# Optimization experiments

Measured on AMD Instinct MI355X. Metric: run time of the kernel, lower is better.

Reference implementation:

```python
import jax, jax.numpy as jnp
import numpy as np

H, KV, D, HID = 32, 8, 128, 4096
B, S = 1, 2048
ROPE_THETA = 10000.0


def setup_inputs() -> dict:
    key = jax.random.key(0)
    ks = jax.random.split(key, 5)
    std = 0.02
    return {
        "x": jax.random.normal(ks[0], (B, S, HID), jnp.float32),
        "Wq": jax.random.normal(ks[1], (H * D, HID), jnp.float32) * std,
        "Wk": jax.random.normal(ks[2], (KV * D, HID), jnp.float32) * std,
        "Wv": jax.random.normal(ks[3], (KV * D, HID), jnp.float32) * std,
        "Wo": jax.random.normal(ks[4], (HID, H * D), jnp.float32) * std,
    }


def _rope_cos_sin(seq_len, dim, dtype):
    inv_freq = 1.0 / (ROPE_THETA ** (jnp.arange(0, dim, 2, dtype=jnp.float32) / dim))
    t = jnp.arange(seq_len, dtype=jnp.float32)
    freqs = jnp.einsum("s,d->sd", t, inv_freq)          # [S, D/2]
    emb = jnp.concatenate([freqs, freqs], axis=-1)        # [S, D]
    return jnp.cos(emb).astype(dtype), jnp.sin(emb).astype(dtype)


def _rotate_half(x):
    x1, x2 = jnp.split(x, 2, axis=-1)
    return jnp.concatenate([-x2, x1], axis=-1)


def reference(x, Wq, Wk, Wv, Wo):
    Bx, Sx, _ = x.shape
    q = (x @ Wq.T).reshape(Bx, Sx, H, D).transpose(0, 2, 1, 3)    # [B,H,S,D]
    k = (x @ Wk.T).reshape(Bx, Sx, KV, D).transpose(0, 2, 1, 3)   # [B,KV,S,D]
    v = (x @ Wv.T).reshape(Bx, Sx, KV, D).transpose(0, 2, 1, 3)

    cos, sin = _rope_cos_sin(Sx, D, x.dtype)                       # [S,D]
    q = q * cos + _rotate_half(q) * sin
    k = k * cos + _rotate_half(k) * sin

    rep = H // KV
    k = jnp.repeat(k, rep, axis=1)                                 # [B,H,S,D]
    v = jnp.repeat(v, rep, axis=1)

    scale = 1.0 / jnp.sqrt(jnp.asarray(D, x.dtype))
    scores = jnp.einsum("bhqd,bhkd->bhqk", q, k) * scale           # [B,H,S,S]
    causal = jnp.tril(jnp.ones((Sx, Sx), dtype=bool))
    scores = jnp.where(causal, scores, jnp.asarray(-1e30, x.dtype))
    attn = jax.nn.softmax(scores, axis=-1)
    out = jnp.einsum("bhqk,bhkd->bhqd", attn, v)                   # [B,H,S,D]
    out = out.transpose(0, 2, 1, 3).reshape(Bx, Sx, H * D)
    return out @ Wo.T
```

## Files before the change

kernel.cpp:

```cpp
#include <hip/hip_runtime.h>

typedef unsigned short u16;
typedef unsigned int u32;

using f32x4  = __attribute__((ext_vector_type(4))) float;
using f32x16 = __attribute__((ext_vector_type(16))) float;
using bf16x8 = __attribute__((ext_vector_type(8))) __bf16;

#define S_LEN 2048
#define HID_DIM 4096
#define NH 32
#define NKV 8
#define HD 128
#define QKVN 6144

__device__ __forceinline__ u16 f2b(float f) {
  union { float f; u32 u; } v; v.f = f;
  u32 r = (v.u + 0x7FFFu + ((v.u >> 16) & 1u)) >> 16;
  return (u16)r;
}
__device__ __forceinline__ float b2f(u16 b) {
  union { u32 u; float f; } v; v.u = ((u32)b) << 16;
  return v.f;
}

__device__ __forceinline__ u32 cvtpk_bf16(float lo, float hi) {
  u32 r;
  asm("v_cvt_pk_bf16_f32 %0, %1, %2" : "=v"(r) : "v"(lo), "v"(hi));
  return r;
}
__device__ __forceinline__ void plane_swap(u32& a, u32& b) {
  asm volatile("v_permlane32_swap_b32 %0, %1" : "+v"(a), "+v"(b));
}

#define AS1 __attribute__((address_space(1)))
#define AS3 __attribute__((address_space(3)))
__device__ __forceinline__ void gl_lds16(const u16* g, u16* l) {
  __builtin_amdgcn_global_load_lds((const AS1 u32*)g, (AS3 u32*)l, 16, 0, 0);
}

#define SBAR  __builtin_amdgcn_s_barrier()
#define SCHED0 __builtin_amdgcn_sched_barrier(0)
#define LGKM0 do { asm volatile("s_waitcnt lgkmcnt(0)" ::: "memory"); SCHED0; } while (0)
#define PRIO1 __builtin_amdgcn_s_setprio(1)
#define PRIO0 __builtin_amdgcn_s_setprio(0)

template <int N> __device__ __forceinline__ void waitv() {
  if constexpr (N == 0)      asm volatile("s_waitcnt vmcnt(0)" ::: "memory");
  else if constexpr (N == 4) asm volatile("s_waitcnt vmcnt(4)" ::: "memory");
  else if constexpr (N == 5) asm volatile("s_waitcnt vmcnt(5)" ::: "memory");
  else if constexpr (N == 6) asm volatile("s_waitcnt vmcnt(6)" ::: "memory");
  else if constexpr (N == 7) asm volatile("s_waitcnt vmcnt(7)" ::: "memory");
  else                       asm volatile("s_waitcnt vmcnt(0)" ::: "memory");
  SCHED0;
}

#define X4T 2097152
#define Q4T 4194304
#define K4T 1048576
#define TOT4 (X4T + Q4T + K4T + K4T + Q4T)
__global__ void cast_all(const float* __restrict__ x,  const float* __restrict__ wq,
                         const float* __restrict__ wk, const float* __restrict__ wv,
                         const float* __restrict__ wo,
                         u16* __restrict__ xb, u16* __restrict__ wqkv,
                         u16* __restrict__ wo_b) {
  int i = blockIdx.x * blockDim.x + threadIdx.x;
  int stride = gridDim.x * blockDim.x;
  for (; i < TOT4; i += stride) {
    const float* src;
    uint2* dst;
    int off;
    if (i < X4T)                     { src = x;  dst = (uint2*)xb;   off = i; }
    else if (i < X4T + Q4T)          { src = wq; dst = (uint2*)wqkv; off = i - X4T; }
    else if (i < X4T + Q4T + K4T)    { src = wk; dst = (uint2*)wqkv + Q4T; off = i - X4T - Q4T; }
    else if (i < X4T + Q4T + 2*K4T)  { src = wv; dst = (uint2*)wqkv + Q4T + K4T; off = i - X4T - Q4T - K4T; }
    else                             { src = wo; dst = (uint2*)wo_b; off = i - X4T - Q4T - 2*K4T; }
    float4 v = ((const float4*)src)[off];
    uint2 o;
    o.x = (u32)f2b(v.x) | ((u32)f2b(v.y) << 16);
    o.y = (u32)f2b(v.z) | ((u32)f2b(v.w) << 16);
    dst[off] = o;
  }
}

#define STAGE(DST, SRC, CH, LDK)                                   \
  _Pragma("unroll") for (int c = 0; c < (CH); ++c) {               \
    int d_ = c * 8192 + tid * 16;                                  \
    int rw_ = d_ >> 7;                                             \
    int cb_ = (d_ & 127) ^ ((rw_ & 7) << 4);                       \
    gl_lds16((SRC) + (size_t)rw_ * (LDK) + (cb_ >> 1), (DST) + (d_ >> 1)); \
  }

#define RDA(ABUF, MLO, KS)                                                    \
  _Pragma("unroll") for (int mm = 0; mm < 4; ++mm)                            \
    af[(MLO) + mm][KS] = *(const bf16x8*)((const char*)(ABUF) +               \
      (wmo + ((MLO) + mm) * 16 + lr) * 128 + (((((KS) << 2) | lg) ^ lr7) << 4));

#define RDB(BBUF, KS)                                                         \
  _Pragma("unroll") for (int nn = 0; nn < NF; ++nn)                           \
    bfr[nn][KS] = *(const bf16x8*)((const char*)(BBUF) +                      \
      (wno + nn * 16 + lr) * 128 + (((((KS) << 2) | lg) ^ lr7) << 4));

#define MFMA_Q(MLO, KS)                                                       \
  _Pragma("unroll") for (int mm = 0; mm < 4; ++mm)                            \
  _Pragma("unroll") for (int nn = 0; nn < NF; ++nn)                           \
    acc[(MLO) + mm][nn] = __builtin_amdgcn_mfma_f32_16x16x32_bf16(            \
        af[(MLO) + mm][KS], bfr[nn][KS], acc[(MLO) + mm][nn], 0, 0, 0);

template <int BM, int BN, int WN, int CBF>
__global__ __launch_bounds__(512, 4) void gemm8p(
    const u16* __restrict__ A, const u16* __restrict__ B, void* __restrict__ Cout,
    int M, int N, int K)
{
  constexpr int MF = BM / 32;
  constexpr int NF = WN / 16;
  constexpr int LA = BM / 64;
  constexpr int LB = BN / 64;
  constexpr int LT = LA + LB;
  extern __shared__ __align__(16) u16 smem[];
  u16* const As0 = smem;
  u16* const Bs0 = smem + 2 * BM * 64;

  const int tid  = threadIdx.x;
  const int lane = tid & 63;
  const int wave = tid >> 6;
  const int lr  = lane & 15;
  const int lg  = lane >> 4;
  const int lr7 = lane & 7;

  const int nbx = N / BN;
  const int bid = blockIdx.x;
  const int cpx = gridDim.x >> 3;
  const int swz = (bid & 7) * cpx + (bid >> 3);
  const int bm = (swz / nbx) * BM;
  const int bn = (swz % nbx) * BN;
  const int wmo = (wave >> 2) * (BM / 2);
  const int wno = (wave & 3) * WN;

  const int NT = K >> 6;

  f32x4 acc[MF][NF] = {};
  bf16x8 af[MF][2], bfr[NF][2];

  const u16* aP = A + (size_t)bm * K;
  const u16* bP = B + (size_t)bn * K;

  STAGE(As0,           aP,      LA, K);
  STAGE(Bs0,           bP,      LB, K);
  STAGE(As0 + BM * 64, aP + 64, LA, K);
  STAGE(Bs0 + BN * 64, bP + 64, LB, K);
  waitv<LT>();
  SBAR; SCHED0;

  for (int t = 0; t < NT; ++t) {
    const int buf = t & 1;
    const u16* ab = As0 + buf * (BM * 64);
    const u16* bb = Bs0 + buf * (BN * 64);
    const bool st = (t + 2 < NT);

    RDA(ab, 0, 0);
    if constexpr (MF == 8) { RDA(ab, 4, 0); }
    RDB(bb, 0);
    LGKM0;
    PRIO1; MFMA_Q(0, 0); if constexpr (MF == 8) { MFMA_Q(4, 0); } PRIO0;
    RDA(ab, 0, 1);
    if constexpr (MF == 8) { RDA(ab, 4, 1); }
    RDB(bb, 1);
    LGKM0;
    SBAR;

    if (st) {
      STAGE(As0 + buf * (BM * 64), aP + (size_t)(t + 2) * 64, LA, K);
      STAGE(Bs0 + buf * (BN * 64), bP + (size_t)(t + 2) * 64, LB, K);
    }
    PRIO1; MFMA_Q(0, 1); if constexpr (MF == 8) { MFMA_Q(4, 1); } PRIO0;
    if (t + 1 < NT) {
      if (st) waitv<LT>(); else waitv<0>();
    }
    SBAR; SCHED0;
  }

#pragma unroll
  for (int m = 0; m < MF; ++m)
#pragma unroll
    for (int j = 0; j < 4; ++j) {
      int row = bm + wmo + m * 16 + lg * 4 + j;
      size_t base = (size_t)row * N + bn + wno + lr;
      if constexpr (CBF) {
        u16* C = (u16*)Cout;
#pragma unroll
        for (int nn = 0; nn < NF; ++nn) C[base + nn * 16] = f2b(acc[m][nn][j]);
      } else {
        float* C = (float*)Cout;
#pragma unroll
        for (int nn = 0; nn < NF; ++nn) C[base + nn * 16] = acc[m][nn][j];
      }
    }
}

__global__ void rope_qk(const u16* __restrict__ qkv, u16* __restrict__ dst,
                        int col_off, float scale, int frag) {
  int idx = blockIdx.x * blockDim.x + threadIdx.x;
  int i = idx & 63;
  int s = (idx >> 6) & (S_LEN - 1);
  int h = idx >> 17;
  const u16* row = qkv + (size_t)s * QKVN + col_off + h * HD;
  float a = b2f(row[i]);
  float b = b2f(row[i + 64]);
  float invf = __expf(-(float)i * 0.14391156831212787f);
  float f = (float)s * invf;
  float sn, cs;
  sincosf(f, &sn, &cs);
  float o1 = (a * cs - b * sn) * scale;
  float o2 = (b * cs + a * sn) * scale;
  if (frag) {
    int qt = h * 64 + (s >> 5);
    int qq = s & 31;
    int i2 = i + 64;
    dst[((qt * 8 + (i  >> 4)) * 2 + ((i  >> 3) & 1)) * 256 + qq * 8 + (i  & 7)] = f2b(o1);
    dst[((qt * 8 + (i2 >> 4)) * 2 + ((i2 >> 3) & 1)) * 256 + qq * 8 + (i2 & 7)] = f2b(o2);
  } else {
    u16* orow = dst + ((size_t)h * S_LEN + s) * HD;
    orow[i]      = f2b(o1);
    orow[i + 64] = f2b(o2);
  }
}

__global__ __launch_bounds__(256) void vf_pack(const u16* __restrict__ qkv,
                                               u16* __restrict__ VF) {
  __shared__ u16 vlds[32][136];
  const int bid = blockIdx.x;
  const int kv = bid >> 6, t = bid & 63;
  const int tid = threadIdx.x;
  const int r = tid >> 3, d0 = (tid & 7) * 16;
  const u16* src = qkv + (size_t)(t * 32 + r) * QKVN + 5120 + kv * HD + d0;
  *(bf16x8*)&vlds[r][d0]     = *(const bf16x8*)src;
  *(bf16x8*)&vlds[r][d0 + 8] = *(const bf16x8*)(src + 8);
  __syncthreads();
  u16* outt = VF + (size_t)bid * 4096;
#pragma unroll
  for (int g = 0; g < 2; ++g) {
    int G = tid + g * 256;
    int q = G & 31, dt = (G >> 5) & 3, hi2 = (G >> 7) & 1, kc = G >> 8;
    union { u16 u[8]; uint4 v; } o;
#pragma unroll
    for (int e = 0; e < 8; ++e)
      o.u[e] = vlds[kc * 16 + hi2 * 8 + e][dt * 32 + q];
    *(uint4*)&outt[G * 8] = o.v;
  }
}

__global__ __launch_bounds__(256, 2) void attn_fwd(
    const u16* __restrict__ QF,
    const u16* __restrict__ KF,
    const u16* __restrict__ VF,
    u16* __restrict__ Out)
{
  const int tid  = threadIdx.x;
  const int lane = tid & 63;
  const int wv   = tid >> 6;
  const int q31  = lane & 31;
  const int hi   = lane >> 5;
  const int bid  = blockIdx.x;
  const int kvh  = bid & 7;
  const int qi   = 63 - (bid >> 3);
  const int q0   = qi * 32;
  const int h    = kvh * 4 + wv;
  const int nt   = qi + 1;

  const u16* kbase = KF + (size_t)kvh * 64 * 4096 + hi * 256  + q31 * 8;
  const u16* vbase = VF + (size_t)kvh * 64 * 4096 + hi * 1024 + q31 * 8;

  bf16x8 qf[8];
  const u16* qfp = QF + (size_t)(h * 64 + qi) * 4096 + hi * 256 + q31 * 8;
#pragma unroll
  for (int dc = 0; dc < 8; ++dc)
    qf[dc] = *(const bf16x8*)(qfp + dc * 512);

  f32x16 o0 = {}, o1 = {}, o2 = {}, o3 = {};
  float m = -1e30f, lsum = 0.f;

  for (int t = 0; t < nt; ++t) {
    SBAR;

    bf16x8 kf[8];
    const u16* kfp = kbase + (size_t)t * 4096;
#pragma unroll
    for (int dc = 0; dc < 8; ++dc)
      kf[dc] = *(const bf16x8*)(kfp + dc * 512);

    bf16x8 vf[8];
    const u16* vfp = vbase + (size_t)t * 4096;
#pragma unroll
    for (int i = 0; i < 8; ++i)
      vf[i] = *(const bf16x8*)(vfp + (i & 1) * 2048 + (i >> 1) * 256);

    f32x16 st = {};
    PRIO1;
#pragma unroll
    for (int dc = 0; dc < 8; ++dc)
      st = __builtin_amdgcn_mfma_f32_32x32x16_bf16(kf[dc], qf[dc], st, 0, 0, 0);
    PRIO0;

    if (t == nt - 1) {
#pragma unroll
      for (int r = 0; r < 16; ++r) {
        int kk = (r & 3) + 8 * (r >> 2) + 4 * hi;
        if (kk > q31) st[r] = -1e30f;
      }
    }

    float a0 = fmaxf(st[0], st[1]),   a1 = fmaxf(st[2], st[3]);
    float a2 = fmaxf(st[4], st[5]),   a3 = fmaxf(st[6], st[7]);
    float a4 = fmaxf(st[8], st[9]),   a5 = fmaxf(st[10], st[11]);
    float a6 = fmaxf(st[12], st[13]), a7 = fmaxf(st[14], st[15]);
    a0 = fmaxf(a0, a1); a2 = fmaxf(a2, a3); a4 = fmaxf(a4, a5); a6 = fmaxf(a6, a7);
    float pmax = fmaxf(fmaxf(a0, a2), fmaxf(a4, a6));
    pmax = fmaxf(pmax, __shfl_xor(pmax, 32));

    if (__any(pmax > m + 8.f)) {
      float mn = fmaxf(m, pmax);
      float sf = exp2f(m - mn);
      m = mn;
      lsum *= sf;
#pragma unroll
      for (int r = 0; r < 16; ++r) { o0[r] *= sf; o1[r] *= sf; o2[r] *= sf; o3[r] *= sf; }
    }

    float ev[16];
#pragma unroll
    for (int r = 0; r < 16; ++r) ev[r] = exp2f(st[r] - m);
    float s0 = (ev[0] + ev[1]) + (ev[2] + ev[3]);
    float s1 = (ev[4] + ev[5]) + (ev[6] + ev[7]);
    float s2 = (ev[8] + ev[9]) + (ev[10] + ev[11]);
    float s3 = (ev[12] + ev[13]) + (ev[14] + ev[15]);
    float ps = (s0 + s1) + (s2 + s3);
    ps += __shfl_xor(ps, 32);
    lsum += ps;

    u32 c0 = cvtpk_bf16(ev[0],  ev[1]),  c1 = cvtpk_bf16(ev[2],  ev[3]);
    u32 c2 = cvtpk_bf16(ev[4],  ev[5]),  c3 = cvtpk_bf16(ev[6],  ev[7]);
    u32 c4 = cvtpk_bf16(ev[8],  ev[9]),  c5 = cvtpk_bf16(ev[10], ev[11]);
    u32 c6 = cvtpk_bf16(ev[12], ev[13]), c7 = cvtpk_bf16(ev[14], ev[15]);
    plane_swap(c0, c2);
    plane_swap(c1, c3);
    plane_swap(c4, c6);
    plane_swap(c5, c7);
    union { u32 u[4]; bf16x8 v; } pb0u, pb1u;
    pb0u.u[0] = c0; pb0u.u[1] = c1; pb0u.u[2] = c2; pb0u.u[3] = c3;
    pb1u.u[0] = c4; pb1u.u[1] = c5; pb1u.u[2] = c6; pb1u.u[3] = c7;

    PRIO1;
    o0 = __builtin_amdgcn_mfma_f32_32x32x16_bf16(vf[0], pb0u.v, o0, 0, 0, 0);
    o1 = __builtin_amdgcn_mfma_f32_32x32x16_bf16(vf[2], pb0u.v, o1, 0, 0, 0);
    o2 = __builtin_amdgcn_mfma_f32_32x32x16_bf16(vf[4], pb0u.v, o2, 0, 0, 0);
    o3 = __builtin_amdgcn_mfma_f32_32x32x16_bf16(vf[6], pb0u.v, o3, 0, 0, 0);
    o0 = __builtin_amdgcn_mfma_f32_32x32x16_bf16(vf[1], pb1u.v, o0, 0, 0, 0);
    o1 = __builtin_amdgcn_mfma_f32_32x32x16_bf16(vf[3], pb1u.v, o1, 0, 0, 0);
    o2 = __builtin_amdgcn_mfma_f32_32x32x16_bf16(vf[5], pb1u.v, o2, 0, 0, 0);
    o3 = __builtin_amdgcn_mfma_f32_32x32x16_bf16(vf[7], pb1u.v, o3, 0, 0, 0);
    PRIO0;
  }

  float inv = 1.0f / lsum;
  u16* orow = Out + (size_t)(q0 + q31) * (NH * HD) + h * HD;
#pragma unroll
  for (int dt = 0; dt < 4; ++dt) {
    const f32x16& oo = dt == 0 ? o0 : dt == 1 ? o1 : dt == 2 ? o2 : o3;
#pragma unroll
    for (int g = 0; g < 4; ++g) {
      ushort4 pk;
      pk.x = f2b(oo[g * 4 + 0] * inv);
      pk.y = f2b(oo[g * 4 + 1] * inv);
      pk.z = f2b(oo[g * 4 + 2] * inv);
      pk.w = f2b(oo[g * 4 + 3] * inv);
      *(ushort4*)&orow[dt * 32 + 8 * g + 4 * hi] = pk;
    }
  }
}

extern "C" void kernel_launch(void* const* d_in, const int* in_sizes, int n_in,
                              void* d_out, int out_size, void* d_ws, size_t ws_size,
                              hipStream_t stream) {
  const float* x  = (const float*)d_in[0];
  const float* Wq = (const float*)d_in[1];
  const float* Wk = (const float*)d_in[2];
  const float* Wv = (const float*)d_in[3];
  const float* Wo = (const float*)d_in[4];
  float* out = (float*)d_out;

  char* ws = (char*)d_ws;
  u16* xb   = (u16*)(ws);
  u16* wqkv = (u16*)(ws + (16ull << 20));
  u16* wo_b = (u16*)(ws + (64ull << 20));
  u16* qkvb = (u16*)(ws + (96ull << 20));
  u16* qb   = (u16*)(ws + (16ull << 20));
  u16* kfb  = (u16*)(ws + (32ull << 20));
  u16* vfb  = (u16*)(ws + (36ull << 20));
  u16* ao   = (u16*)(ws);

  const int smem_q = (128 + 192) * 64 * 2 * 2;
  const int smem_o = (128 + 128) * 64 * 2 * 2;
  hipFuncSetAttribute((const void*)&gemm8p<128, 192, 48, 1>,
                      hipFuncAttributeMaxDynamicSharedMemorySize, smem_q);
  hipFuncSetAttribute((const void*)&gemm8p<128, 128, 32, 0>,
                      hipFuncAttributeMaxDynamicSharedMemorySize, smem_o);

  cast_all<<<4096, 256, 0, stream>>>(x, Wq, Wk, Wv, Wo, xb, wqkv, wo_b);

  gemm8p<128, 192, 48, 1><<<512, 512, smem_q, stream>>>(xb, wqkv, qkvb, 2048, 6144, 4096);

  rope_qk<<<(32 * 2048 * 64) / 256, 256, 0, stream>>>(qkvb, qb,  0,    0.12751741f, 1);
  rope_qk<<<(8  * 2048 * 64) / 256, 256, 0, stream>>>(qkvb, kfb, 4096, 1.0f,        1);
  vf_pack<<<512, 256, 0, stream>>>(qkvb, vfb);

  attn_fwd<<<512, 256, 0, stream>>>(qb, kfb, vfb, ao);

  gemm8p<128, 128, 32, 0><<<512, 512, smem_o, stream>>>(ao, wo_b, out, 2048, 4096, 4096);
}
```

Before: 337.6 us.

## Pre-swizzle weights into MFMA fragment layout and read B directly from global

```diff
diff --git a/kernel.cpp b/kernel.cpp
--- a/kernel.cpp
+++ b/kernel.cpp
@@ -47,10 +47,8 @@
 
 template <int N> __device__ __forceinline__ void waitv() {
   if constexpr (N == 0)      asm volatile("s_waitcnt vmcnt(0)" ::: "memory");
+  else if constexpr (N == 2) asm volatile("s_waitcnt vmcnt(2)" ::: "memory");
   else if constexpr (N == 4) asm volatile("s_waitcnt vmcnt(4)" ::: "memory");
-  else if constexpr (N == 5) asm volatile("s_waitcnt vmcnt(5)" ::: "memory");
-  else if constexpr (N == 6) asm volatile("s_waitcnt vmcnt(6)" ::: "memory");
-  else if constexpr (N == 7) asm volatile("s_waitcnt vmcnt(7)" ::: "memory");
   else                       asm volatile("s_waitcnt vmcnt(0)" ::: "memory");
   SCHED0;
 }
@@ -59,27 +57,37 @@
 #define Q4T 4194304
 #define K4T 1048576
 #define TOT4 (X4T + Q4T + K4T + K4T + Q4T)
+__device__ __forceinline__ void frag_store(u16* base, int n, int k0, uint2 o) {
+  int F = n >> 4, lr = n & 15, c = k0 >> 5, lg = (k0 >> 3) & 3, e0 = k0 & 7;
+  *(uint2*)&base[((((size_t)F * 128 + c) * 4 + lg) * 128) + lr * 8 + e0] = o;
+}
 __global__ void cast_all(const float* __restrict__ x,  const float* __restrict__ wq,
                          const float* __restrict__ wk, const float* __restrict__ wv,
                          const float* __restrict__ wo,
-                         u16* __restrict__ xb, u16* __restrict__ wqkv,
-                         u16* __restrict__ wo_b) {
+                         u16* __restrict__ xb, u16* __restrict__ wqkvF,
+                         u16* __restrict__ woF) {
   int i = blockIdx.x * blockDim.x + threadIdx.x;
   int stride = gridDim.x * blockDim.x;
   for (; i < TOT4; i += stride) {
     const float* src;
-    uint2* dst;
-    int off;
-    if (i < X4T)                     { src = x;  dst = (uint2*)xb;   off = i; }
-    else if (i < X4T + Q4T)          { src = wq; dst = (uint2*)wqkv; off = i - X4T; }
-    else if (i < X4T + Q4T + K4T)    { src = wk; dst = (uint2*)wqkv + Q4T; off = i - X4T - Q4T; }
-    else if (i < X4T + Q4T + 2*K4T)  { src = wv; dst = (uint2*)wqkv + Q4T + K4T; off = i - X4T - Q4T - K4T; }
-    else                             { src = wo; dst = (uint2*)wo_b; off = i - X4T - Q4T - 2*K4T; }
+    int off, mode, nbias = 0;
+    u16* base;
+    if (i < X4T)                     { src = x;  off = i;                     mode = 0; base = xb; }
+    else if (i < X4T + Q4T)          { src = wq; off = i - X4T;               mode = 1; base = wqkvF; }
+    else if (i < X4T + Q4T + K4T)    { src = wk; off = i - X4T - Q4T;         mode = 1; base = wqkvF; nbias = 4096; }
+    else if (i < X4T + Q4T + 2*K4T)  { src = wv; off = i - X4T - Q4T - K4T;   mode = 1; base = wqkvF; nbias = 5120; }
+    else                             { src = wo; off = i - X4T - Q4T - 2*K4T; mode = 1; base = woF; }
     float4 v = ((const float4*)src)[off];
     uint2 o;
     o.x = (u32)f2b(v.x) | ((u32)f2b(v.y) << 16);
     o.y = (u32)f2b(v.z) | ((u32)f2b(v.w) << 16);
-    dst[off] = o;
+    if (mode == 0) {
+      ((uint2*)base)[off] = o;
+    } else {
+      int n = (off >> 10) + nbias;
+      int k0 = (off & 1023) * 4;
+      frag_store(base, n, k0, o);
+    }
   }
 }
 
@@ -91,35 +99,32 @@
     gl_lds16((SRC) + (size_t)rw_ * (LDK) + (cb_ >> 1), (DST) + (d_ >> 1)); \
   }
 
-#define RDA(ABUF, MLO, KS)                                                    \
+#define RDA(ABUF, KS)                                                         \
   _Pragma("unroll") for (int mm = 0; mm < 4; ++mm)                            \
-    af[(MLO) + mm][KS] = *(const bf16x8*)((const char*)(ABUF) +               \
-      (wmo + ((MLO) + mm) * 16 + lr) * 128 + (((((KS) << 2) | lg) ^ lr7) << 4));
-
-#define RDB(BBUF, KS)                                                         \
+    af[mm][KS] = *(const bf16x8*)((const char*)(ABUF) +                       \
+      (wmo + mm * 16 + lr) * 128 + (((((KS) << 2) | lg) ^ lr7) << 4));
+
+#define RDBG(T, KS)                                                           \
   _Pragma("unroll") for (int nn = 0; nn < NF; ++nn)                           \
-    bfr[nn][KS] = *(const bf16x8*)((const char*)(BBUF) +                      \
-      (wno + nn * 16 + lr) * 128 + (((((KS) << 2) | lg) ^ lr7) << 4));
-
-#define MFMA_Q(MLO, KS)                                                       \
+    bfr[nn][KS] = *(const bf16x8*)&BF[((((size_t)(nF0 + nn) * (K >> 5) +      \
+      ((T) * 2 + (KS))) * 4 + lg) << 7) + lr * 8];
+
+#define MFMA_Q(KS)                                                            \
   _Pragma("unroll") for (int mm = 0; mm < 4; ++mm)                            \
   _Pragma("unroll") for (int nn = 0; nn < NF; ++nn)                           \
-    acc[(MLO) + mm][nn] = __builtin_amdgcn_mfma_f32_16x16x32_bf16(            \
-        af[(MLO) + mm][KS], bfr[nn][KS], acc[(MLO) + mm][nn], 0, 0, 0);
-
-template <int BM, int BN, int WN, int CBF>
-__global__ __launch_bounds__(512, 4) void gemm8p(
-    const u16* __restrict__ A, const u16* __restrict__ B, void* __restrict__ Cout,
+    acc[mm][nn] = __builtin_amdgcn_mfma_f32_16x16x32_bf16(                    \
+        af[mm][KS], bfr[nn][KS], acc[mm][nn], 0, 0, 0);
+
+template <int BN, int WN, int CBF>
+__global__ __launch_bounds__(512, 2) void gemm_bg(
+    const u16* __restrict__ A, const u16* __restrict__ BF, void* __restrict__ Cout,
     int M, int N, int K)
 {
-  constexpr int MF = BM / 32;
   constexpr int NF = WN / 16;
-  constexpr int LA = BM / 64;
-  constexpr int LB = BN / 64;
-  constexpr int LT = LA + LB;
+  constexpr int BM = 128;
+  constexpr int LA = 2;
   extern __shared__ __align__(16) u16 smem[];
   u16* const As0 = smem;
-  u16* const Bs0 = smem + 2 * BM * 64;
 
   const int tid  = threadIdx.x;
   const int lane = tid & 63;
@@ -134,54 +139,44 @@
   const int swz = (bid & 7) * cpx + (bid >> 3);
   const int bm = (swz / nbx) * BM;
   const int bn = (swz % nbx) * BN;
-  const int wmo = (wave >> 2) * (BM / 2);
+  const int wmo = (wave >> 2) * 64;
   const int wno = (wave & 3) * WN;
+  const int nF0 = (bn + wno) >> 4;
 
   const int NT = K >> 6;
 
-  f32x4 acc[MF][NF] = {};
-  bf16x8 af[MF][2], bfr[NF][2];
+  f32x4 acc[4][NF] = {};
+  bf16x8 af[4][2], bfr[NF][2];
 
   const u16* aP = A + (size_t)bm * K;
-  const u16* bP = B + (size_t)bn * K;
-
-  STAGE(As0,           aP,      LA, K);
-  STAGE(Bs0,           bP,      LB, K);
-  STAGE(As0 + BM * 64, aP + 64, LA, K);
-  STAGE(Bs0 + BN * 64, bP + 64, LB, K);
-  waitv<LT>();
+
+  STAGE(As0,        aP,      LA, K);
+  STAGE(As0 + 8192, aP + 64, LA, K);
+  waitv<2>();
   SBAR; SCHED0;
 
   for (int t = 0; t < NT; ++t) {
     const int buf = t & 1;
-    const u16* ab = As0 + buf * (BM * 64);
-    const u16* bb = Bs0 + buf * (BN * 64);
+    const u16* ab = As0 + buf * 8192;
     const bool st = (t + 2 < NT);
 
-    RDA(ab, 0, 0);
-    if constexpr (MF == 8) { RDA(ab, 4, 0); }
-    RDB(bb, 0);
+    RDA(ab, 0); RDBG(t, 0);
     LGKM0;
-    PRIO1; MFMA_Q(0, 0); if constexpr (MF == 8) { MFMA_Q(4, 0); } PRIO0;
-    RDA(ab, 0, 1);
-    if constexpr (MF == 8) { RDA(ab, 4, 1); }
-    RDB(bb, 1);
+    PRIO1; MFMA_Q(0); PRIO0;
+    RDA(ab, 1); RDBG(t, 1);
     LGKM0;
     SBAR;
 
-    if (st) {
-      STAGE(As0 + buf * (BM * 64), aP + (size_t)(t + 2) * 64, LA, K);
-      STAGE(Bs0 + buf * (BN * 64), bP + (size_t)(t + 2) * 64, LB, K);
-    }
-    PRIO1; MFMA_Q(0, 1); if constexpr (MF == 8) { MFMA_Q(4, 1); } PRIO0;
+    if (st) { STAGE(As0 + buf * 8192, aP + (size_t)(t + 2) * 64, LA, K); }
+    PRIO1; MFMA_Q(1); PRIO0;
     if (t + 1 < NT) {
-      if (st) waitv<LT>(); else waitv<0>();
+      if (st) waitv<2>(); else waitv<0>();
     }
     SBAR; SCHED0;
   }
 
 #pragma unroll
-  for (int m = 0; m < MF; ++m)
+  for (int m = 0; m < 4; ++m)
 #pragma unroll
     for (int j = 0; j < 4; ++j) {
       int row = bm + wmo + m * 16 + lg * 4 + j;
@@ -390,25 +385,24 @@
   float* out = (float*)d_out;
 
   char* ws = (char*)d_ws;
-  u16* xb   = (u16*)(ws);
-  u16* wqkv = (u16*)(ws + (16ull << 20));
-  u16* wo_b = (u16*)(ws + (64ull << 20));
-  u16* qkvb = (u16*)(ws + (96ull << 20));
-  u16* qb   = (u16*)(ws + (16ull << 20));
-  u16* kfb  = (u16*)(ws + (32ull << 20));
-  u16* vfb  = (u16*)(ws + (36ull << 20));
-  u16* ao   = (u16*)(ws);
-
-  const int smem_q = (128 + 192) * 64 * 2 * 2;
-  const int smem_o = (128 + 128) * 64 * 2 * 2;
-  hipFuncSetAttribute((const void*)&gemm8p<128, 192, 48, 1>,
-                      hipFuncAttributeMaxDynamicSharedMemorySize, smem_q);
-  hipFuncSetAttribute((const void*)&gemm8p<128, 128, 32, 0>,
-                      hipFuncAttributeMaxDynamicSharedMemorySize, smem_o);
-
-  cast_all<<<4096, 256, 0, stream>>>(x, Wq, Wk, Wv, Wo, xb, wqkv, wo_b);
-
-  gemm8p<128, 192, 48, 1><<<512, 512, smem_q, stream>>>(xb, wqkv, qkvb, 2048, 6144, 4096);
+  u16* xb    = (u16*)(ws);
+  u16* wqkvF = (u16*)(ws + (16ull << 20));
+  u16* woF   = (u16*)(ws + (64ull << 20));
+  u16* qkvb  = (u16*)(ws + (96ull << 20));
+  u16* qb    = (u16*)(ws + (16ull << 20));
+  u16* kfb   = (u16*)(ws + (32ull << 20));
+  u16* vfb   = (u16*)(ws + (36ull << 20));
+  u16* ao    = (u16*)(ws);
+
+  const int smem_g = 2 * 128 * 64 * 2;
+  hipFuncSetAttribute((const void*)&gemm_bg<192, 48, 1>,
+                      hipFuncAttributeMaxDynamicSharedMemorySize, smem_g);
+  hipFuncSetAttribute((const void*)&gemm_bg<128, 32, 0>,
+                      hipFuncAttributeMaxDynamicSharedMemorySize, smem_g);
+
+  cast_all<<<4096, 256, 0, stream>>>(x, Wq, Wk, Wv, Wo, xb, wqkvF, woF);
+
+  gemm_bg<192, 48, 1><<<512, 512, smem_g, stream>>>(xb, wqkvF, qkvb, 2048, 6144, 4096);
 
   rope_qk<<<(32 * 2048 * 64) / 256, 256, 0, stream>>>(qkvb, qb,  0,    0.12751741f, 1);
   rope_qk<<<(8  * 2048 * 64) / 256, 256, 0, stream>>>(qkvb, kfb, 4096, 1.0f,        1);
@@ -416,5 +410,5 @@
 
   attn_fwd<<<512, 256, 0, stream>>>(qb, kfb, vfb, ao);
 
-  gemm8p<128, 128, 32, 0><<<512, 512, smem_o, stream>>>(ao, wo_b, out, 2048, 4096, 4096);
-}
+  gemm_bg<128, 32, 0><<<512, 512, smem_g, stream>>>(ao, woF, out, 2048, 4096, 4096);
+}
```

Result: slower. 426.1 us (+26.2%).
